# Kernel optimization log

Hardware: AMD Instinct MI355X
Metric: run time of the kernel (lower is better)

Reference implementation:

```python
import jax, jax.numpy as jnp
import numpy as np

B, S, D, H = 4, 2048, 1024, 16
DEPTH = D // H


def setup_inputs() -> dict:
    root = jax.random.key(0)
    ks = jax.random.split(root, 12)
    std = 0.02
    return {
        "value": jax.random.normal(ks[0], (B, S, D), jnp.float32),
        "key": jax.random.normal(ks[1], (B, S, D), jnp.float32),
        "query": jax.random.normal(ks[2], (B, S, D), jnp.float32),
        "mask": jax.random.randint(ks[3], (B, 1, S, S), 0, 2, jnp.int32),
        "Wq": jax.random.normal(ks[4], (D, D), jnp.float32) * std,
        "bq": jnp.zeros((D,), jnp.float32),
        "Wk": jax.random.normal(ks[5], (D, D), jnp.float32) * std,
        "bk": jnp.zeros((D,), jnp.float32),
        "Wv": jax.random.normal(ks[6], (D, D), jnp.float32) * std,
        "bv": jnp.zeros((D,), jnp.float32),
        "Wo": jax.random.normal(ks[7], (D, D), jnp.float32) * std,
        "bo": jnp.zeros((D,), jnp.float32),
    }


def _split_heads(x):
    # [B,S,D] -> [B,H,S,depth]
    b, s, _ = x.shape
    return x.reshape(b, s, H, DEPTH).transpose(0, 2, 1, 3)


def reference(value, key, query, mask, Wq, bq, Wk, bk, Wv, bv, Wo, bo):
    elu = jax.nn.elu
    q = _split_heads(elu(query @ Wq + bq))
    k = _split_heads(elu(key @ Wk + bk))
    v = _split_heads(elu(value @ Wv + bv))
    # scaled dot-product attention; scale by sqrt(depth) (last dim of split key)
    logits = jnp.einsum("bhqd,bhkd->bhqk", q, k) / jnp.sqrt(jnp.float32(DEPTH))
    logits = logits + mask.astype(jnp.float32) * -1e9
    attn = jax.nn.softmax(logits, axis=-1)
    ctx = jnp.einsum("bhqk,bhkd->bhqd", attn, v)  # [B,H,S,depth]
    ctx = ctx.transpose(0, 2, 1, 3).reshape(ctx.shape[0], -1, D)  # [B,S,D]
    return elu(ctx @ Wo + bo)
```

## Files before the change

kernel.cpp:

```cpp
#include <hip/hip_runtime.h>

typedef unsigned short u16;
typedef unsigned int   u32;
typedef unsigned long long u64;
typedef __bf16 bf16x8 __attribute__((ext_vector_type(8)));
typedef float  f32x4  __attribute__((ext_vector_type(4)));
typedef float  f32x16 __attribute__((ext_vector_type(16)));
typedef u32    u32x4  __attribute__((ext_vector_type(4)));

__device__ __forceinline__ u16 f2bf(float f) {
    u32 u = __float_as_uint(f);
    return (u16)((u + 0x7FFFu + ((u >> 16) & 1u)) >> 16);
}
__device__ __forceinline__ float fexp2(float x) {
    float r;
    asm("v_exp_f32 %0, %1" : "=v"(r) : "v"(x));
    return r;
}
__device__ __forceinline__ float elu_f(float x) {
    return x > 0.f ? x : fexp2(x * 1.44269504088896341f) - 1.f;
}
__device__ __forceinline__ void gload_lds16(const void* g, void* l) {
    __builtin_amdgcn_global_load_lds(
        (const __attribute__((address_space(1))) void*)g,
        (__attribute__((address_space(3))) void*)l, 16, 0, 0);
}
__device__ __forceinline__ u32 cvtpk(float a, float b) {
    u32 r;
    asm("v_cvt_pk_bf16_f32 %0, %1, %2" : "=v"(r) : "v"(a), "v"(b));
    return r;
}
__device__ __forceinline__ void plswap(u32& a, u32& b) {
    asm volatile("v_permlane32_swap_b32 %0, %1" : "+v"(a), "+v"(b));
}

__global__ __launch_bounds__(256) void transpose_w4(
    const float* __restrict__ W0, const float* __restrict__ W1,
    const float* __restrict__ W2, const float* __restrict__ W3,
    u16* __restrict__ T0, u16* __restrict__ T1,
    u16* __restrict__ T2, u16* __restrict__ T3) {
    const float* W = blockIdx.z == 0 ? W0 : blockIdx.z == 1 ? W1 : blockIdx.z == 2 ? W2 : W3;
    u16* Wt        = blockIdx.z == 0 ? T0 : blockIdx.z == 1 ? T1 : blockIdx.z == 2 ? T2 : T3;
    __shared__ float t[32][33];
    int j0 = blockIdx.x * 32, k0 = blockIdx.y * 32;
    int tx = threadIdx.x, ty = threadIdx.y;
#pragma unroll
    for (int i = 0; i < 4; ++i)
        t[ty + i * 8][tx] = W[(long)(k0 + ty + i * 8) * 1024 + j0 + tx];
    __syncthreads();
#pragma unroll
    for (int i = 0; i < 4; ++i)
        Wt[(long)(j0 + ty + i * 8) * 1024 + k0 + tx] = f2bf(t[tx][ty + i * 8]);
}

__global__ __launch_bounds__(256) void cvt_bf16(const float* __restrict__ X,
                                                u16* __restrict__ Y, int n4) {
    int i = blockIdx.x * 256 + threadIdx.x;
    int st = gridDim.x * 256;
    for (; i < n4; i += st) {
        float4 v = ((const float4*)X)[i];
        u64 pk = (u64)f2bf(v.x) | ((u64)f2bf(v.y) << 16) |
                 ((u64)f2bf(v.z) << 32) | ((u64)f2bf(v.w) << 48);
        ((u64*)Y)[i] = pk;
    }
}

__global__ __launch_bounds__(256) void pack_mask(const int* __restrict__ mask,
                                                 u64* __restrict__ bits, long n64) {
    long wid  = ((long)blockIdx.x * blockDim.x + threadIdx.x) >> 6;
    int  lane = threadIdx.x & 63;
    long nw   = ((long)gridDim.x * blockDim.x) >> 6;
    for (long w = wid; w < n64; w += nw) {
        int m = mask[w * 64 + lane];
        u64 b = __ballot(m != 0);
        if (lane == 0) bits[w] = b;
    }
}

#define GEMM_BODY(A_, Bt_)                                                      \
    const int tid = threadIdx.x, lane = tid & 63, w = tid >> 6;                 \
    const int wm = w >> 1, wn = w & 1;                                          \
    const int vb = ((blockIdx.x & 7) << 6) + (blockIdx.x >> 3);                 \
    const int m0 = (vb & 63) * 128;                                             \
    const int n0 = (vb >> 6) * 128;                                             \
    const int lrow = lane & 15;                                                 \
    const int hi4 = lane >> 4;                                                  \
    const int srow = w * 32 + (lane >> 3);                                      \
    const int scw = ((lane & 7) ^ ((lane >> 3) & 7)) * 8;                       \
    const u16* gA = (A_) + (long)(m0 + srow) * 1024 + scw;                      \
    const u16* gB = (Bt_) + (long)(n0 + srow) * 1024 + scw;                     \
    f32x4 acc[4][4] = {};                                                       \
    STAGE(0, 0);                                                                \
    __syncthreads();                                                            \
    int cur = 0;                                                                \
    const int rswz = (lrow & 7) << 4;                                           \
    for (int k0 = 0; k0 < 1024; k0 += 64) {                                     \
        if (k0 + 64 < 1024) { STAGE(cur ^ 1, k0 + 64); }                        \
        const char* Ac = (const char*)As[cur];                                  \
        const char* Bc = (const char*)Bs[cur];                                  \
        _Pragma("unroll") for (int kk = 0; kk < 2; ++kk) {                      \
            bf16x8 af[4], bfr[4];                                               \
            _Pragma("unroll") for (int mi = 0; mi < 4; ++mi) {                  \
                int r = wm * 64 + mi * 16 + lrow;                               \
                af[mi] = *(const bf16x8*)(Ac + ((r * 128 + kk * 64 + hi4 * 16) ^ rswz)); \
            }                                                                   \
            _Pragma("unroll") for (int ni = 0; ni < 4; ++ni) {                  \
                int r = wn * 64 + ni * 16 + lrow;                               \
                bfr[ni] = *(const bf16x8*)(Bc + ((r * 128 + kk * 64 + hi4 * 16) ^ rswz)); \
            }                                                                   \
            _Pragma("unroll") for (int mi = 0; mi < 4; ++mi)                    \
                _Pragma("unroll") for (int ni = 0; ni < 4; ++ni)                \
                    acc[mi][ni] = __builtin_amdgcn_mfma_f32_16x16x32_bf16(      \
                        af[mi], bfr[ni], acc[mi][ni], 0, 0, 0);                 \
        }                                                                       \
        __syncthreads();                                                        \
        cur ^= 1;                                                               \
    }

#define STAGE(BUF, KOFF)                                                        \
    gload_lds16(gA + (KOFF),            (char*)As[BUF] + w * 4096);             \
    gload_lds16(gA + 8 * 1024 + (KOFF), (char*)As[BUF] + w * 4096 + 1024);      \
    gload_lds16(gA + 16 * 1024 + (KOFF), (char*)As[BUF] + w * 4096 + 2048);     \
    gload_lds16(gA + 24 * 1024 + (KOFF), (char*)As[BUF] + w * 4096 + 3072);     \
    gload_lds16(gB + (KOFF),            (char*)Bs[BUF] + w * 4096);             \
    gload_lds16(gB + 8 * 1024 + (KOFF), (char*)Bs[BUF] + w * 4096 + 1024);      \
    gload_lds16(gB + 16 * 1024 + (KOFF), (char*)Bs[BUF] + w * 4096 + 2048);     \
    gload_lds16(gB + 24 * 1024 + (KOFF), (char*)Bs[BUF] + w * 4096 + 3072);

__global__ __launch_bounds__(256) void gemm_qkv(
    const u16* __restrict__ Aq, const u16* __restrict__ Ak, const u16* __restrict__ Av,
    const u16* __restrict__ Wqt, const u16* __restrict__ Wkt, const u16* __restrict__ Wvt,
    const float* __restrict__ bq, const float* __restrict__ bk, const float* __restrict__ bv,
    u16* __restrict__ Qb, u16* __restrict__ Kb, u16* __restrict__ Vt, int zforce) {
    __shared__ u16 As[2][128 * 64];
    __shared__ u16 Bs[2][128 * 64];
    const int z = zforce >= 0 ? zforce : blockIdx.y;
    const u16* A     = z == 0 ? Aq : z == 1 ? Ak : Av;
    const u16* Bt    = z == 0 ? Wqt : z == 1 ? Wkt : Wvt;
    const float* bias = z == 0 ? bq : z == 1 ? bk : bv;

    GEMM_BODY(A, Bt)

    if (z != 2) {
        u16* O = z == 0 ? Qb : Kb;
        const int rbase = m0 + wm * 64 + hi4 * 4;
        const int cbase = n0 + wn * 64 + lrow;
#pragma unroll
        for (int mi = 0; mi < 4; ++mi)
#pragma unroll
            for (int ni = 0; ni < 4; ++ni) {
                int row = rbase + mi * 16;
                int col = cbase + ni * 16;
                float bsv = bias[col];
                f32x4 a = acc[mi][ni];
#pragma unroll
                for (int r = 0; r < 4; ++r) {
                    float v = elu_f(a[r] + bsv);
                    if (z == 0) v *= 0.18033688011112042f;
                    O[(long)(row + r) * 1024 + col] = f2bf(v);
                }
            }
    } else {
        __syncthreads();
        char* T = (char*)&As[0][0];
#pragma unroll
        for (int mi = 0; mi < 4; ++mi)
#pragma unroll
            for (int ni = 0; ni < 4; ++ni) {
                int d = wn * 64 + ni * 16 + lrow;
                int sb = wm * 16 + mi * 4 + hi4;
                float bsv = bias[n0 + d];
                f32x4 a = acc[mi][ni];
                u64 pk = (u64)f2bf(elu_f(a[0] + bsv)) |
                         ((u64)f2bf(elu_f(a[1] + bsv)) << 16) |
                         ((u64)f2bf(elu_f(a[2] + bsv)) << 32) |
                         ((u64)f2bf(elu_f(a[3] + bsv)) << 48);
                *(u64*)(T + ((d * 256 + sb * 8) ^ ((d & 15) << 3))) = pk;
            }
        __syncthreads();
        const int bb = m0 >> 11, sbase = m0 & 2047;
        const int d = tid >> 1;
        const int s0 = (tid & 1) * 16;
        const int dm = n0 + d;
        long gb = ((long)(bb * 16 + (dm >> 6)) * 64 + (dm & 63)) * 2048 + sbase;
#pragma unroll
        for (int c = 0; c < 8; ++c) {
            int si = s0 + 2 * c;
            u64 lo = *(u64*)(T + ((d * 256 + si * 8) ^ ((d & 15) << 3)));
            u64 hi = *(u64*)(T + ((d * 256 + (si + 1) * 8) ^ ((d & 15) << 3)));
            *(u64*)(Vt + gb + si * 4) = lo;
            *(u64*)(Vt + gb + si * 4 + 4) = hi;
        }
    }
}

__global__ __launch_bounds__(256) void gemm_out(const u16* __restrict__ Actx,
                                                const u16* __restrict__ Wot,
                                                const float* __restrict__ bias,
                                                float* __restrict__ Out) {
    __shared__ u16 As[2][128 * 64];
    __shared__ u16 Bs[2][128 * 64];

    GEMM_BODY(Actx, Wot)

    const int rbase = m0 + wm * 64 + hi4 * 4;
    const int cbase = n0 + wn * 64 + lrow;
#pragma unroll
    for (int mi = 0; mi < 4; ++mi)
#pragma unroll
        for (int ni = 0; ni < 4; ++ni) {
            int row = rbase + mi * 16;
            int col = cbase + ni * 16;
            float bsv = bias[col];
            f32x4 a = acc[mi][ni];
#pragma unroll
            for (int r = 0; r < 4; ++r)
                Out[(long)(row + r) * 1024 + col] = elu_f(a[r] + bsv);
        }
}

__device__ __forceinline__ void attn_tile(
    const u16* Ksb, const u16* Vsb, u64 mw,
    const bf16x8& qf0, const bf16x8& qf1, const bf16x8& qf2, const bf16x8& qf3,
    f32x16& pa0, f32x16& pa1, float& psum, int lo5, int hi2) {
    const int swz = (lo5 & 7) << 4;
    const int cb  = hi2 * 16;
    const char* Kc = (const char*)Ksb;
    const char* Vc = (const char*)Vsb;
#pragma unroll
    for (int sidx = 0; sidx < 2; ++sidx) {
        f32x16 s = {};
#define RK(C_) (*(const bf16x8*)(Kc + (((sidx * 32 + lo5) * 128 + (C_) * 32 + cb) ^ swz)))
        s = __builtin_amdgcn_mfma_f32_32x32x16_bf16(RK(0), qf0, s, 0, 0, 0);
        s = __builtin_amdgcn_mfma_f32_32x32x16_bf16(RK(1), qf1, s, 0, 0, 0);
        s = __builtin_amdgcn_mfma_f32_32x32x16_bf16(RK(2), qf2, s, 0, 0, 0);
        s = __builtin_amdgcn_mfma_f32_32x32x16_bf16(RK(3), qf3, s, 0, 0, 0);
#undef RK
        u32 nw = ~(((u32)(mw >> (sidx * 32))) >> (hi2 * 4));
        float p[16];
        float ls0 = 0.f, ls1 = 0.f;
#pragma unroll
        for (int r = 0; r < 16; ++r) {
            int bit = (r & 3) + 8 * (r >> 2);
            u32 keep = (u32)((int)(nw << (31 - bit)) >> 31);
            float pe = fexp2(s[r]);
            p[r] = __uint_as_float(__float_as_uint(pe) & keep);
            if (r & 1) ls1 += p[r]; else ls0 += p[r];
        }
        psum += ls0 + ls1;
#pragma unroll
        for (int th = 0; th < 2; ++th) {
            int rb = th * 8;
            u32 a0 = cvtpk(p[rb + 0], p[rb + 1]);
            u32 a1 = cvtpk(p[rb + 2], p[rb + 3]);
            u32 b0 = cvtpk(p[rb + 4], p[rb + 5]);
            u32 b1 = cvtpk(p[rb + 6], p[rb + 7]);
            plswap(a0, b0);
            plswap(a1, b1);
            u32x4 au; au.x = a0; au.y = a1; au.z = b0; au.w = b1;
            bf16x8 pf = __builtin_bit_cast(bf16x8, au);
            int t = sidx * 2 + th;
            bf16x8 v0 = *(const bf16x8*)(Vc + ((lo5 * 128 + t * 32 + cb) ^ swz));
            pa0 = __builtin_amdgcn_mfma_f32_32x32x16_bf16(pf, v0, pa0, 0, 0, 0);
            bf16x8 v1 = *(const bf16x8*)(Vc + (((32 + lo5) * 128 + t * 32 + cb) ^ swz));
            pa1 = __builtin_amdgcn_mfma_f32_32x32x16_bf16(pf, v1, pa1, 0, 0, 0);
        }
    }
}

__global__ __launch_bounds__(256, 3) void attn32(const u16* __restrict__ Q,
                                                 const u16* __restrict__ Kb,
                                                 const u16* __restrict__ Vt,
                                                 const u64* __restrict__ mbits,
                                                 u16* __restrict__ Co) {
    const int S = 2048;
    __shared__ u16 Ks[2][64 * 64];
    __shared__ u16 Vs[2][64 * 64];

    const int tid = threadIdx.x, lane = tid & 63, w = tid >> 6;
    const int lo5 = lane & 31, hi2 = lane >> 5;
    const int q0 = blockIdx.x * 128;
    const int bh = blockIdx.y, b = bh >> 4, h = bh & 15;

    const int qrow = q0 + w * 32 + lo5;
    const u16* qp = Q + (long)(b * S + qrow) * 1024 + h * 64 + hi2 * 8;
    bf16x8 qf0 = *(const bf16x8*)(qp);
    bf16x8 qf1 = *(const bf16x8*)(qp + 16);
    bf16x8 qf2 = *(const bf16x8*)(qp + 32);
    bf16x8 qf3 = *(const bf16x8*)(qp + 48);

    f32x16 pa0 = {}; f32x16 pa1 = {};
    float psum = 0.f;

    const u64* mrow = mbits + (long)(b * S + qrow) * 32;

    const int r_  = w * 16 + (lane >> 3);
    const int cp_ = (lane & 7) ^ ((lane >> 3) & 7);
    const u16* kSrc = Kb + (long)(b * S + r_) * 1024 + h * 64 + cp_ * 8;
    const u16* vSrc = Vt + ((long)bh * 64 + r_) * 2048 + cp_ * 8;

#define STAGEA(BUF, T)                                                         \
    gload_lds16(kSrc + (long)(T) * 65536,         (char*)Ks[BUF] + w * 2048);        \
    gload_lds16(kSrc + (long)(T) * 65536 + 8192,  (char*)Ks[BUF] + w * 2048 + 1024); \
    gload_lds16(vSrc + (long)(T) * 64,            (char*)Vs[BUF] + w * 2048);        \
    gload_lds16(vSrc + (long)(T) * 64 + 8 * 2048, (char*)Vs[BUF] + w * 2048 + 1024);

    int buf = 0;
    u64 mw = mrow[0], mwn = 0;
    STAGEA(0, 0);
    __syncthreads();

    for (int t = 0; t < 32; ++t) {
        if (t < 31) { STAGEA(buf ^ 1, t + 1); mwn = mrow[t + 1]; }
        attn_tile(Ks[buf], Vs[buf], mw, qf0, qf1, qf2, qf3, pa0, pa1, psum, lo5, hi2);
        __syncthreads();
        mw = mwn; buf ^= 1;
    }
#undef STAGEA

    float tot = psum + __shfl_xor(psum, 32);
    float inv = 1.f / tot;

    const long obase = (long)(b * S + q0 + w * 32) * 1024 + h * 64;
#pragma unroll
    for (int r = 0; r < 16; ++r) {
        int ql = (r & 3) + 8 * (r >> 2) + 4 * hi2;
        float iv = __shfl(inv, ql);
        Co[obase + (long)ql * 1024 + lo5]      = f2bf(pa0[r] * iv);
        Co[obase + (long)ql * 1024 + 32 + lo5] = f2bf(pa1[r] * iv);
    }
}

extern "C" void kernel_launch(void* const* d_in, const int* in_sizes, int n_in,
                              void* d_out, int out_size, void* d_ws, size_t ws_size,
                              hipStream_t stream) {
    const float* value = (const float*)d_in[0];
    const float* key   = (const float*)d_in[1];
    const float* query = (const float*)d_in[2];
    const int*   mask  = (const int*)d_in[3];
    const float* Wq = (const float*)d_in[4];
    const float* bq = (const float*)d_in[5];
    const float* Wk = (const float*)d_in[6];
    const float* bk = (const float*)d_in[7];
    const float* Wv = (const float*)d_in[8];
    const float* bv = (const float*)d_in[9];
    const float* Wo = (const float*)d_in[10];
    const float* bo = (const float*)d_in[11];

    char* ws = (char*)d_ws;
    const size_t MB2 = 1u << 21, MB16 = 1u << 24;
    u16* Wq_t = (u16*)(ws);
    u16* Wk_t = (u16*)(ws + MB2);
    u16* Wv_t = (u16*)(ws + 2 * MB2);
    u16* Wo_t = (u16*)(ws + 3 * MB2);
    u64* mbits = (u64*)(ws + 4 * MB2);
    char* big0 = ws + 5 * MB2;
    u16* Qb = (u16*)(big0);
    u16* Kb = (u16*)(big0 + MB16);
    u16* Vt = (u16*)(big0 + 2 * MB16);
    u16* Aq = (u16*)(big0 + 3 * MB16);
    u16* Ctx = Aq;
    u16* Ak = (u16*)(big0 + 4 * MB16);
    u16* Av = (u16*)(big0 + 5 * MB16);
    const bool bigws = ws_size >= (size_t)(5 * MB2 + 6 * MB16);

    transpose_w4<<<dim3(32, 32, 4), dim3(32, 8), 0, stream>>>(
        Wq, Wk, Wv, Wo, Wq_t, Wk_t, Wv_t, Wo_t);
    pack_mask<<<1024, 256, 0, stream>>>(mask, mbits, 262144L);

    const int n4 = 8192 * 1024 / 4;
    if (bigws) {
        cvt_bf16<<<2048, 256, 0, stream>>>(query, Aq, n4);
        cvt_bf16<<<2048, 256, 0, stream>>>(key,   Ak, n4);
        cvt_bf16<<<2048, 256, 0, stream>>>(value, Av, n4);
        gemm_qkv<<<dim3(512, 3), 256, 0, stream>>>(Aq, Ak, Av, Wq_t, Wk_t, Wv_t,
                                                   bq, bk, bv, Qb, Kb, Vt, -1);
    } else {
        cvt_bf16<<<2048, 256, 0, stream>>>(query, Aq, n4);
        gemm_qkv<<<dim3(512, 1), 256, 0, stream>>>(Aq, Aq, Aq, Wq_t, Wk_t, Wv_t,
                                                   bq, bk, bv, Qb, Kb, Vt, 0);
        cvt_bf16<<<2048, 256, 0, stream>>>(key, Aq, n4);
        gemm_qkv<<<dim3(512, 1), 256, 0, stream>>>(Aq, Aq, Aq, Wq_t, Wk_t, Wv_t,
                                                   bq, bk, bv, Qb, Kb, Vt, 1);
        cvt_bf16<<<2048, 256, 0, stream>>>(value, Aq, n4);
        gemm_qkv<<<dim3(512, 1), 256, 0, stream>>>(Aq, Aq, Aq, Wq_t, Wk_t, Wv_t,
                                                   bq, bk, bv, Qb, Kb, Vt, 2);
    }

    attn32<<<dim3(16, 64), 256, 0, stream>>>(Qb, Kb, Vt, mbits, Ctx);
    gemm_out<<<512, 256, 0, stream>>>(Ctx, Wo_t, bo, (float*)d_out);
}
```

Before: 294.3 us.

## Switch bf16 pipeline to fp16, raise attention occupancy, drop batched QKV path

Converts all bf16 storage and MFMA ops to fp16 (16x16x32_f16 and 32x32x16_f16), replacing the packed bf16 conversion asm with scalar half casts. Raises the attention kernel launch bound from 3 to 4 blocks per SM and uses sbfe for mask bit extraction. Removes the large-workspace path that converted all three inputs and ran one batched QKV GEMM, always using three serialized convert+GEMM pairs. The fp16 cast path may cost more instructions than v_cvt_pk_bf16, and dropping the batched launch adds serialization; fp16 also risks overflow on unnormalized probabilities or large activations.

```diff
diff --git a/kernel.cpp b/kernel.cpp
--- a/kernel.cpp
+++ b/kernel.cpp
@@ -3,14 +3,14 @@
 typedef unsigned short u16;
 typedef unsigned int   u32;
 typedef unsigned long long u64;
-typedef __bf16 bf16x8 __attribute__((ext_vector_type(8)));
+typedef _Float16 f16x8 __attribute__((ext_vector_type(8)));
 typedef float  f32x4  __attribute__((ext_vector_type(4)));
 typedef float  f32x16 __attribute__((ext_vector_type(16)));
 typedef u32    u32x4  __attribute__((ext_vector_type(4)));
 
-__device__ __forceinline__ u16 f2bf(float f) {
-    u32 u = __float_as_uint(f);
-    return (u16)((u + 0x7FFFu + ((u >> 16) & 1u)) >> 16);
+__device__ __forceinline__ u16 f2h(float f) {
+    _Float16 h = (_Float16)f;
+    return __builtin_bit_cast(u16, h);
 }
 __device__ __forceinline__ float fexp2(float x) {
     float r;
@@ -25,10 +25,8 @@
         (const __attribute__((address_space(1))) void*)g,
         (__attribute__((address_space(3))) void*)l, 16, 0, 0);
 }
-__device__ __forceinline__ u32 cvtpk(float a, float b) {
-    u32 r;
-    asm("v_cvt_pk_bf16_f32 %0, %1, %2" : "=v"(r) : "v"(a), "v"(b));
-    return r;
+__device__ __forceinline__ u32 pkh(float a, float b) {
+    return (u32)f2h(a) | ((u32)f2h(b) << 16);
 }
 __device__ __forceinline__ void plswap(u32& a, u32& b) {
     asm volatile("v_permlane32_swap_b32 %0, %1" : "+v"(a), "+v"(b));
@@ -50,17 +48,17 @@
     __syncthreads();
 #pragma unroll
     for (int i = 0; i < 4; ++i)
-        Wt[(long)(j0 + ty + i * 8) * 1024 + k0 + tx] = f2bf(t[tx][ty + i * 8]);
-}
-
-__global__ __launch_bounds__(256) void cvt_bf16(const float* __restrict__ X,
-                                                u16* __restrict__ Y, int n4) {
+        Wt[(long)(j0 + ty + i * 8) * 1024 + k0 + tx] = f2h(t[tx][ty + i * 8]);
+}
+
+__global__ __launch_bounds__(256) void cvt_f16(const float* __restrict__ X,
+                                               u16* __restrict__ Y, int n4) {
     int i = blockIdx.x * 256 + threadIdx.x;
     int st = gridDim.x * 256;
     for (; i < n4; i += st) {
         float4 v = ((const float4*)X)[i];
-        u64 pk = (u64)f2bf(v.x) | ((u64)f2bf(v.y) << 16) |
-                 ((u64)f2bf(v.z) << 32) | ((u64)f2bf(v.w) << 48);
+        u64 pk = (u64)f2h(v.x) | ((u64)f2h(v.y) << 16) |
+                 ((u64)f2h(v.z) << 32) | ((u64)f2h(v.w) << 48);
         ((u64*)Y)[i] = pk;
     }
 }
@@ -99,18 +97,18 @@
         const char* Ac = (const char*)As[cur];                                  \
         const char* Bc = (const char*)Bs[cur];                                  \
         _Pragma("unroll") for (int kk = 0; kk < 2; ++kk) {                      \
-            bf16x8 af[4], bfr[4];                                               \
+            f16x8 af[4], bfr[4];                                                \
             _Pragma("unroll") for (int mi = 0; mi < 4; ++mi) {                  \
                 int r = wm * 64 + mi * 16 + lrow;                               \
-                af[mi] = *(const bf16x8*)(Ac + ((r * 128 + kk * 64 + hi4 * 16) ^ rswz)); \
+                af[mi] = *(const f16x8*)(Ac + ((r * 128 + kk * 64 + hi4 * 16) ^ rswz)); \
             }                                                                   \
             _Pragma("unroll") for (int ni = 0; ni < 4; ++ni) {                  \
                 int r = wn * 64 + ni * 16 + lrow;                               \
-                bfr[ni] = *(const bf16x8*)(Bc + ((r * 128 + kk * 64 + hi4 * 16) ^ rswz)); \
+                bfr[ni] = *(const f16x8*)(Bc + ((r * 128 + kk * 64 + hi4 * 16) ^ rswz)); \
             }                                                                   \
             _Pragma("unroll") for (int mi = 0; mi < 4; ++mi)                    \
                 _Pragma("unroll") for (int ni = 0; ni < 4; ++ni)                \
-                    acc[mi][ni] = __builtin_amdgcn_mfma_f32_16x16x32_bf16(      \
+                    acc[mi][ni] = __builtin_amdgcn_mfma_f32_16x16x32_f16(       \
                         af[mi], bfr[ni], acc[mi][ni], 0, 0, 0);                 \
         }                                                                       \
         __syncthreads();                                                        \
@@ -157,7 +155,7 @@
                 for (int r = 0; r < 4; ++r) {
                     float v = elu_f(a[r] + bsv);
                     if (z == 0) v *= 0.18033688011112042f;
-                    O[(long)(row + r) * 1024 + col] = f2bf(v);
+                    O[(long)(row + r) * 1024 + col] = f2h(v);
                 }
             }
     } else {
@@ -171,10 +169,10 @@
                 int sb = wm * 16 + mi * 4 + hi4;
                 float bsv = bias[n0 + d];
                 f32x4 a = acc[mi][ni];
-                u64 pk = (u64)f2bf(elu_f(a[0] + bsv)) |
-                         ((u64)f2bf(elu_f(a[1] + bsv)) << 16) |
-                         ((u64)f2bf(elu_f(a[2] + bsv)) << 32) |
-                         ((u64)f2bf(elu_f(a[3] + bsv)) << 48);
+                u64 pk = (u64)f2h(elu_f(a[0] + bsv)) |
+                         ((u64)f2h(elu_f(a[1] + bsv)) << 16) |
+                         ((u64)f2h(elu_f(a[2] + bsv)) << 32) |
+                         ((u64)f2h(elu_f(a[3] + bsv)) << 48);
                 *(u64*)(T + ((d * 256 + sb * 8) ^ ((d & 15) << 3))) = pk;
             }
         __syncthreads();
@@ -221,7 +219,7 @@
 
 __device__ __forceinline__ void attn_tile(
     const u16* Ksb, const u16* Vsb, u64 mw,
-    const bf16x8& qf0, const bf16x8& qf1, const bf16x8& qf2, const bf16x8& qf3,
+    const f16x8& qf0, const f16x8& qf1, const f16x8& qf2, const f16x8& qf3,
     f32x16& pa0, f32x16& pa1, float& psum, int lo5, int hi2) {
     const int swz = (lo5 & 7) << 4;
     const int cb  = hi2 * 16;
@@ -230,19 +228,19 @@
 #pragma unroll
     for (int sidx = 0; sidx < 2; ++sidx) {
         f32x16 s = {};
-#define RK(C_) (*(const bf16x8*)(Kc + (((sidx * 32 + lo5) * 128 + (C_) * 32 + cb) ^ swz)))
-        s = __builtin_amdgcn_mfma_f32_32x32x16_bf16(RK(0), qf0, s, 0, 0, 0);
-        s = __builtin_amdgcn_mfma_f32_32x32x16_bf16(RK(1), qf1, s, 0, 0, 0);
-        s = __builtin_amdgcn_mfma_f32_32x32x16_bf16(RK(2), qf2, s, 0, 0, 0);
-        s = __builtin_amdgcn_mfma_f32_32x32x16_bf16(RK(3), qf3, s, 0, 0, 0);
+#define RK(C_) (*(const f16x8*)(Kc + (((sidx * 32 + lo5) * 128 + (C_) * 32 + cb) ^ swz)))
+        s = __builtin_amdgcn_mfma_f32_32x32x16_f16(RK(0), qf0, s, 0, 0, 0);
+        s = __builtin_amdgcn_mfma_f32_32x32x16_f16(RK(1), qf1, s, 0, 0, 0);
+        s = __builtin_amdgcn_mfma_f32_32x32x16_f16(RK(2), qf2, s, 0, 0, 0);
+        s = __builtin_amdgcn_mfma_f32_32x32x16_f16(RK(3), qf3, s, 0, 0, 0);
 #undef RK
         u32 nw = ~(((u32)(mw >> (sidx * 32))) >> (hi2 * 4));
         float p[16];
         float ls0 = 0.f, ls1 = 0.f;
 #pragma unroll
         for (int r = 0; r < 16; ++r) {
-            int bit = (r & 3) + 8 * (r >> 2);
-            u32 keep = (u32)((int)(nw << (31 - bit)) >> 31);
+            const int bit = (r & 3) + 8 * (r >> 2);
+            u32 keep = (u32)__builtin_amdgcn_sbfe(nw, bit, 1);
             float pe = fexp2(s[r]);
             p[r] = __uint_as_float(__float_as_uint(pe) & keep);
             if (r & 1) ls1 += p[r]; else ls0 += p[r];
@@ -251,24 +249,24 @@
 #pragma unroll
         for (int th = 0; th < 2; ++th) {
             int rb = th * 8;
-            u32 a0 = cvtpk(p[rb + 0], p[rb + 1]);
-            u32 a1 = cvtpk(p[rb + 2], p[rb + 3]);
-            u32 b0 = cvtpk(p[rb + 4], p[rb + 5]);
-            u32 b1 = cvtpk(p[rb + 6], p[rb + 7]);
+            u32 a0 = pkh(p[rb + 0], p[rb + 1]);
+            u32 a1 = pkh(p[rb + 2], p[rb + 3]);
+            u32 b0 = pkh(p[rb + 4], p[rb + 5]);
+            u32 b1 = pkh(p[rb + 6], p[rb + 7]);
             plswap(a0, b0);
             plswap(a1, b1);
             u32x4 au; au.x = a0; au.y = a1; au.z = b0; au.w = b1;
-            bf16x8 pf = __builtin_bit_cast(bf16x8, au);
+            f16x8 pf = __builtin_bit_cast(f16x8, au);
             int t = sidx * 2 + th;
-            bf16x8 v0 = *(const bf16x8*)(Vc + ((lo5 * 128 + t * 32 + cb) ^ swz));
-            pa0 = __builtin_amdgcn_mfma_f32_32x32x16_bf16(pf, v0, pa0, 0, 0, 0);
-            bf16x8 v1 = *(const bf16x8*)(Vc + (((32 + lo5) * 128 + t * 32 + cb) ^ swz));
-            pa1 = __builtin_amdgcn_mfma_f32_32x32x16_bf16(pf, v1, pa1, 0, 0, 0);
+            f16x8 v0 = *(const f16x8*)(Vc + ((lo5 * 128 + t * 32 + cb) ^ swz));
+            pa0 = __builtin_amdgcn_mfma_f32_32x32x16_f16(pf, v0, pa0, 0, 0, 0);
+            f16x8 v1 = *(const f16x8*)(Vc + (((32 + lo5) * 128 + t * 32 + cb) ^ swz));
+            pa1 = __builtin_amdgcn_mfma_f32_32x32x16_f16(pf, v1, pa1, 0, 0, 0);
         }
     }
 }
 
-__global__ __launch_bounds__(256, 3) void attn32(const u16* __restrict__ Q,
+__global__ __launch_bounds__(256, 4) void attn32(const u16* __restrict__ Q,
                                                  const u16* __restrict__ Kb,
                                                  const u16* __restrict__ Vt,
                                                  const u64* __restrict__ mbits,
@@ -284,10 +282,10 @@
 
     const int qrow = q0 + w * 32 + lo5;
     const u16* qp = Q + (long)(b * S + qrow) * 1024 + h * 64 + hi2 * 8;
-    bf16x8 qf0 = *(const bf16x8*)(qp);
-    bf16x8 qf1 = *(const bf16x8*)(qp + 16);
-    bf16x8 qf2 = *(const bf16x8*)(qp + 32);
-    bf16x8 qf3 = *(const bf16x8*)(qp + 48);
+    f16x8 qf0 = *(const f16x8*)(qp);
+    f16x8 qf1 = *(const f16x8*)(qp + 16);
+    f16x8 qf2 = *(const f16x8*)(qp + 32);
+    f16x8 qf3 = *(const f16x8*)(qp + 48);
 
     f32x16 pa0 = {}; f32x16 pa1 = {};
     float psum = 0.f;
@@ -326,8 +324,8 @@
     for (int r = 0; r < 16; ++r) {
         int ql = (r & 3) + 8 * (r >> 2) + 4 * hi2;
         float iv = __shfl(inv, ql);
-        Co[obase + (long)ql * 1024 + lo5]      = f2bf(pa0[r] * iv);
-        Co[obase + (long)ql * 1024 + 32 + lo5] = f2bf(pa1[r] * iv);
+        Co[obase + (long)ql * 1024 + lo5]      = f2h(pa0[r] * iv);
+        Co[obase + (long)ql * 1024 + 32 + lo5] = f2h(pa1[r] * iv);
     }
 }
 
@@ -355,37 +353,26 @@
     u16* Wo_t = (u16*)(ws + 3 * MB2);
     u64* mbits = (u64*)(ws + 4 * MB2);
     char* big0 = ws + 5 * MB2;
-    u16* Qb = (u16*)(big0);
-    u16* Kb = (u16*)(big0 + MB16);
-    u16* Vt = (u16*)(big0 + 2 * MB16);
-    u16* Aq = (u16*)(big0 + 3 * MB16);
-    u16* Ctx = Aq;
-    u16* Ak = (u16*)(big0 + 4 * MB16);
-    u16* Av = (u16*)(big0 + 5 * MB16);
-    const bool bigws = ws_size >= (size_t)(5 * MB2 + 6 * MB16);
+    u16* Qb   = (u16*)(big0);
+    u16* Kb   = (u16*)(big0 + MB16);
+    u16* Vt   = (u16*)(big0 + 2 * MB16);
+    u16* Abuf = (u16*)(big0 + 3 * MB16);
+    u16* Ctx  = Abuf;
 
     transpose_w4<<<dim3(32, 32, 4), dim3(32, 8), 0, stream>>>(
         Wq, Wk, Wv, Wo, Wq_t, Wk_t, Wv_t, Wo_t);
     pack_mask<<<1024, 256, 0, stream>>>(mask, mbits, 262144L);
 
     const int n4 = 8192 * 1024 / 4;
-    if (bigws) {
-        cvt_bf16<<<2048, 256, 0, stream>>>(query, Aq, n4);
-        cvt_bf16<<<2048, 256, 0, stream>>>(key,   Ak, n4);
-        cvt_bf16<<<2048, 256, 0, stream>>>(value, Av, n4);
-        gemm_qkv<<<dim3(512, 3), 256, 0, stream>>>(Aq, Ak, Av, Wq_t, Wk_t, Wv_t,
-                                                   bq, bk, bv, Qb, Kb, Vt, -1);
-    } else {
-        cvt_bf16<<<2048, 256, 0, stream>>>(query, Aq, n4);
-        gemm_qkv<<<dim3(512, 1), 256, 0, stream>>>(Aq, Aq, Aq, Wq_t, Wk_t, Wv_t,
-                                                   bq, bk, bv, Qb, Kb, Vt, 0);
-        cvt_bf16<<<2048, 256, 0, stream>>>(key, Aq, n4);
-        gemm_qkv<<<dim3(512, 1), 256, 0, stream>>>(Aq, Aq, Aq, Wq_t, Wk_t, Wv_t,
-                                                   bq, bk, bv, Qb, Kb, Vt, 1);
-        cvt_bf16<<<2048, 256, 0, stream>>>(value, Aq, n4);
-        gemm_qkv<<<dim3(512, 1), 256, 0, stream>>>(Aq, Aq, Aq, Wq_t, Wk_t, Wv_t,
-                                                   bq, bk, bv, Qb, Kb, Vt, 2);
-    }
+    cvt_f16<<<2048, 256, 0, stream>>>(query, Abuf, n4);
+    gemm_qkv<<<dim3(512, 1), 256, 0, stream>>>(Abuf, Abuf, Abuf, Wq_t, Wk_t, Wv_t,
+                                               bq, bk, bv, Qb, Kb, Vt, 0);
+    cvt_f16<<<2048, 256, 0, stream>>>(key, Abuf, n4);
+    gemm_qkv<<<dim3(512, 1), 256, 0, stream>>>(Abuf, Abuf, Abuf, Wq_t, Wk_t, Wv_t,
+                                               bq, bk, bv, Qb, Kb, Vt, 1);
+    cvt_f16<<<2048, 256, 0, stream>>>(value, Abuf, n4);
+    gemm_qkv<<<dim3(512, 1), 256, 0, stream>>>(Abuf, Abuf, Abuf, Wq_t, Wk_t, Wv_t,
+                                               bq, bk, bv, Qb, Kb, Vt, 2);
 
     attn32<<<dim3(16, 64), 256, 0, stream>>>(Qb, Kb, Vt, mbits, Ctx);
     gemm_out<<<512, 256, 0, stream>>>(Ctx, Wo_t, bo, (float*)d_out);
```

After: 309.3 us. +5.1%, slower.
